# Kernel optimization log

Measured on AMD Instinct MI355X. Metric: run time of the kernel, lower is better.

The kernel has to match this reference:

```python
import jax, jax.numpy as jnp
import numpy as np
from jax import lax

BN_EPS = 1e-5
SQ_EPS = 1e-8


def squash(s, axis=-1):
    # v = (|s|^2 / (1+|s|^2)) * s / |s|
    n2 = jnp.sum(s * s, axis=axis, keepdims=True)
    return (n2 / (1.0 + n2)) * s / jnp.sqrt(n2 + SQ_EPS)


def setup_inputs() -> dict:
    key = jax.random.key(0)
    ks = jax.random.split(key, 5)
    B, C, H, W = 64, 512, 28, 28
    NUM_ROUTES = 8 * 10 * 10  # lower_num_caps * 10 * 10 after k9 s2 conv on 28x28
    features = jax.random.normal(ks[0], (B, C, H, W), jnp.float32)
    conv1_w = jax.random.normal(ks[1], (256, 512, 3, 3), jnp.float32) * 0.02
    conv1_b = jnp.zeros((256,), jnp.float32)
    bn_gamma = jnp.ones((256,), jnp.float32)
    bn_beta = jnp.zeros((256,), jnp.float32)
    bn_mean = jnp.zeros((256,), jnp.float32)
    bn_var = jnp.ones((256,), jnp.float32)
    prim_w = jax.random.normal(ks[2], (256, 256, 9, 9), jnp.float32) * 0.02
    prim_b = jnp.zeros((256,), jnp.float32)
    # routing transform: (num_routes, higher_num_caps, out_dim, in_dim)
    route_w = jax.random.normal(ks[3], (NUM_ROUTES, 2, 16, 32), jnp.float32) * 0.05
    return {"features": features, "conv1_w": conv1_w, "conv1_b": conv1_b,
            "bn_gamma": bn_gamma, "bn_beta": bn_beta, "bn_mean": bn_mean,
            "bn_var": bn_var, "prim_w": prim_w, "prim_b": prim_b,
            "route_w": route_w}


def reference(features, conv1_w, conv1_b, bn_gamma, bn_beta, bn_mean, bn_var,
              prim_w, prim_b, route_w):
    B = features.shape[0]
    dn = ("NCHW", "OIHW", "NCHW")
    # pre_conv: Conv2d(512->256, k3, pad1) + BatchNorm (eval) + ReLU
    x = lax.conv_general_dilated(features, conv1_w, (1, 1), "SAME",
                                 dimension_numbers=dn)
    x = x + conv1_b[None, :, None, None]
    inv = bn_gamma * lax.rsqrt(bn_var + BN_EPS)
    x = x * inv[None, :, None, None] + (bn_beta - bn_mean * inv)[None, :, None, None]
    x = jax.nn.relu(x)
    # primary capsules: Conv2d(256->8*32, k9, s2, valid) -> (B,256,10,10)
    p = lax.conv_general_dilated(x, prim_w, (2, 2), "VALID",
                                 dimension_numbers=dn)
    p = p + prim_b[None, :, None, None]
    Hp, Wp = p.shape[2], p.shape[3]
    # (B, num_caps, cap_dim, Hp*Wp) -> (B, num_caps*Hp*Wp, cap_dim)
    p = p.reshape(B, 8, 32, Hp * Wp).transpose(0, 1, 3, 2).reshape(B, 8 * Hp * Wp, 32)
    lower_caps = squash(p, axis=-1)  # (B, 800, 32)
    # predictions u_hat: (B, routes, higher_caps, out_dim)
    u_hat = jnp.einsum("bri,rjoi->brjo", lower_caps, route_w)
    # dynamic routing-by-agreement
    b = jnp.zeros((B, u_hat.shape[1], u_hat.shape[2]), u_hat.dtype)
    n_iter = 3
    for it in range(n_iter):
        c = jax.nn.softmax(b, axis=2)                  # coupling coeffs
        s = jnp.einsum("brj,brjo->bjo", c, u_hat)      # weighted sum
        v = squash(s, axis=-1)                          # (B, 2, 16)
        if it < n_iter - 1:
            b = b + jnp.einsum("brjo,bjo->brj", u_hat, v)
    return (lower_caps, v)
```

## Files before the change

kernel.cpp:

```cpp
#include <hip/hip_runtime.h>
#include <hip/hip_bf16.h>

#define BN_EPS 1e-5f
#define SQ_EPS 1e-8f

typedef __hip_bfloat16 bf16;
typedef __attribute__((ext_vector_type(8))) short bf16x8;
typedef __attribute__((ext_vector_type(4))) float f32x4;

__device__ __forceinline__ void gload_lds16(const void* g, void* l) {
    __builtin_amdgcn_global_load_lds(
        (const __attribute__((address_space(1))) unsigned int*)g,
        (__attribute__((address_space(3))) unsigned int*)l, 16, 0, 0);
}

__device__ __forceinline__ unsigned short f2bfu(float f) {
    bf16 h = __float2bfloat16(f);
    return *(unsigned short*)&h;
}

__global__ __launch_bounds__(256) void feat_to_nhwc(
    const float* __restrict__ feat, bf16* __restrict__ featP) {
    int b = blockIdx.z, ct = blockIdx.y, pt = blockIdx.x;
    int ci0 = ct * 64, px0 = pt * 64;
    int tid = threadIdx.x;
    __shared__ float t[64][65];
#pragma unroll
    for (int rep = 0; rep < 16; rep++) {
        int ci_l = rep * 4 + (tid >> 6);
        int px = px0 + (tid & 63);
        float v = 0.f;
        if (px < 784) v = feat[(b * 512 + ci0 + ci_l) * 784 + px];
        t[ci_l][tid & 63] = v;
    }
    __syncthreads();
#pragma unroll
    for (int rep = 0; rep < 4; rep++) {
        int px_l = rep * 16 + (tid >> 4);
        int px = px0 + px_l;
        if (px < 784) {
            int h = px / 28, wq = px % 28;
            int ci = (tid & 15) * 4;
            ushort4 o;
            o.x = f2bfu(t[ci + 0][px_l]);
            o.y = f2bfu(t[ci + 1][px_l]);
            o.z = f2bfu(t[ci + 2][px_l]);
            o.w = f2bfu(t[ci + 3][px_l]);
            *(ushort4*)&featP[((b * 30 + h + 1) * 30 + (wq + 1)) * 512 + ci0 + ci] = o;
        }
    }
}

__global__ __launch_bounds__(256) void zero_ring(bf16* __restrict__ featP) {
    int b = blockIdx.x;
    uint4 zz = {0u, 0u, 0u, 0u};
    for (int i = threadIdx.x; i < 116 * 64; i += 256) {
        int rp = i >> 6;
        int ci = (i & 63) * 8;
        int hp, wp;
        if (rp < 30)      { hp = 0;       wp = rp; }
        else if (rp < 60) { hp = 29;      wp = rp - 30; }
        else if (rp < 88) { hp = rp - 59; wp = 0; }
        else              { hp = rp - 87; wp = 29; }
        *(uint4*)&featP[(b * 900 + hp * 30 + wp) * 512 + ci] = zz;
    }
}

__global__ __launch_bounds__(256) void w1F_transform(
    const float* __restrict__ w, bf16* __restrict__ wt1F) {
    int co = blockIdx.x;
    __shared__ float t1[4608];
    const float* src = w + co * 4608;
    for (int i = threadIdx.x; i < 4608; i += 256) t1[i] = src[i];
    __syncthreads();
    int co16 = co >> 4, l15 = co & 15;
    for (int i = threadIdx.x; i < 576; i += 256) {
        int g = i >> 6, cc = (i >> 2) & 15, kq = i & 3;
        short v[8];
#pragma unroll
        for (int j = 0; j < 8; j++) {
            unsigned short u = f2bfu(t1[(cc * 32 + kq * 8 + j) * 9 + g]);
            v[j] = (short)u;
        }
        int fidx = g * 16 + cc;
        bf16x8* dst = (bf16x8*)&wt1F[(fidx * 16 + co16) * 512 + (kq * 16 + l15) * 8];
        bf16x8 pk = {v[0], v[1], v[2], v[3], v[4], v[5], v[6], v[7]};
        *dst = pk;
    }
}

__global__ __launch_bounds__(256) void w2F_transform(
    const float* __restrict__ w, bf16* __restrict__ wt2F) {
    int half = blockIdx.x, co = blockIdx.y;
    __shared__ float t2[10368];
    const float* src = w + co * 20736 + half * 10368;
    for (int i = threadIdx.x; i < 10368; i += 256) t2[i] = src[i];
    __syncthreads();
    int co16 = co >> 4, l15 = co & 15;
    for (int i = threadIdx.x; i < 1296; i += 256) {
        int sh = i >> 4, ccl = (i >> 2) & 3, kq = i & 3;
        int z = sh / 10; if (z > 7) z = 7;
        int s0 = (81 * z) >> 3;
        int fidx = s0 * 8 + (sh - s0) * 8 + (half * 4 + ccl);
        short v[8];
#pragma unroll
        for (int j = 0; j < 8; j++) {
            unsigned short u = f2bfu(t2[(ccl * 32 + kq * 8 + j) * 81 + sh]);
            v[j] = (short)u;
        }
        bf16x8* dst = (bf16x8*)&wt2F[(fidx * 16 + co16) * 512 + (kq * 16 + l15) * 8];
        bf16x8 pk = {v[0], v[1], v[2], v[3], v[4], v[5], v[6], v[7]};
        *dst = pk;
    }
}

__global__ __launch_bounds__(512, 4) void conv1_mfma(
    const bf16* __restrict__ featP, const bf16* __restrict__ wt1F,
    const float* __restrict__ bias, const float* __restrict__ gamma,
    const float* __restrict__ beta, const float* __restrict__ mean,
    const float* __restrict__ var, bf16* __restrict__ x) {
    __shared__ char As4[4 * 7168];
    const int tid = threadIdx.x, lane = tid & 63, w = tid >> 6;
    const int Mt = blockIdx.x;

    const bf16* pA0;
    {
        int r0 = (w << 4) + (lane >> 2);
        int q = (lane & 3) ^ ((r0 >> 1) & 3);
        int m0 = Mt * 112 + (w < 7 ? r0 : 0);
        int b0 = m0 / 784, rr = m0 % 784, h0 = rr / 28, w0 = rr % 28;
        pA0 = featP + ((b0 * 30 + h0) * 30 + w0) * 512 + q * 8;
    }
    const bf16x8* pB = (const bf16x8*)wt1F + w * 128 + lane;

    int a_off[7];
#pragma unroll
    for (int mi = 0; mi < 7; mi++) {
        int r = mi * 16 + (lane & 15);
        a_off[mi] = r * 64 + (((lane >> 4) ^ ((r >> 1) & 3)) * 16);
    }

    f32x4 acc[7][2];
#pragma unroll
    for (int i = 0; i < 7; i++)
#pragma unroll
        for (int j = 0; j < 2; j++) acc[i][j] = f32x4{0.f, 0.f, 0.f, 0.f};

    bf16x8 Bv0[2], Bv1[2];

#define STG1(bi, offE)                                                     \
    do {                                                                   \
        if (w < 7)                                                         \
            gload_lds16(pA0 + (offE), As4 + (bi) * 7168 + w * 1024);       \
    } while (0)

    STG1(0, 0); STG1(1, 32); STG1(2, 64);
    { const bf16x8* bp = pB; Bv0[0] = bp[0]; Bv0[1] = bp[64]; }
    asm volatile("s_waitcnt vmcnt(2)" ::: "memory");
    __builtin_amdgcn_s_barrier();
    asm volatile("" ::: "memory");

#define C1_STEP(u, BU, BL)                                                 \
    do {                                                                   \
        const int t_ = t + (u);                                            \
        const int tt = t_ + 3;                                             \
        {       \
            int g_ = tt >> 4; if (g_ > 8) g_ = 8;                          \
            int cc_ = tt & 15;                                             \
            int ky_ = g_ / 3, kx_ = g_ - 3 * ky_;                          \
            STG1((u + 3) & 3, ky_ * 15360 + kx_ * 512 + cc_ * 32);         \
        }                                                                  \
        {                                                                  \
            int fn = t_ + 1; if (fn > 143) fn = 143;                       \
            const bf16x8* bp = pB + fn * 1024;                             \
            BL[0] = bp[0]; BL[1] = bp[64];                                 \
        }                                                                  \
        const char* Ab = As4 + (u) * 7168;                                 \
        bf16x8 af[7];                                                      \
        _Pragma("unroll")                                                  \
        for (int mi = 0; mi < 7; mi++)                                     \
            af[mi] = *(const bf16x8*)(Ab + a_off[mi]);                     \
        __builtin_amdgcn_s_setprio(1);                                     \
        _Pragma("unroll")                                                  \
        for (int nj = 0; nj < 2; nj++)                                     \
            _Pragma("unroll")                                              \
            for (int mi = 0; mi < 7; mi++)                                 \
                acc[mi][nj] = __builtin_amdgcn_mfma_f32_16x16x32_bf16(     \
                    af[mi], BU[nj], acc[mi][nj], 0, 0, 0);                 \
        __builtin_amdgcn_s_setprio(0);                                     \
        if (t_ < 143) {                                                    \
            asm volatile("s_waitcnt vmcnt(8)" ::: "memory");               \
            __builtin_amdgcn_s_barrier();                                  \
            asm volatile("" ::: "memory");                                 \
        }                                                                  \
    } while (0)

    for (int t = 0; t < 144; t += 4) {
        C1_STEP(0, Bv0, Bv1);
        C1_STEP(1, Bv1, Bv0);
        C1_STEP(2, Bv0, Bv1);
        C1_STEP(3, Bv1, Bv0);
    }

#pragma unroll
    for (int nj = 0; nj < 2; nj++) {
        int co = w * 32 + nj * 16 + (lane & 15);
        float inv = gamma[co] * rsqrtf(var[co] + BN_EPS);
        float sh = beta[co] - mean[co] * inv;
        float bs = bias[co];
#pragma unroll
        for (int mi = 0; mi < 7; mi++) {
            int m0 = Mt * 112 + mi * 16 + ((lane >> 4) << 2);
#pragma unroll
            for (int r = 0; r < 4; r++) {
                float v = (acc[mi][nj][r] + bs) * inv + sh;
                x[(m0 + r) * 256 + co] = __float2bfloat16(fmaxf(v, 0.f));
            }
        }
    }
#undef STG1
#undef C1_STEP
}

__global__ __launch_bounds__(512, 4) void conv2_mfma(
    const bf16* __restrict__ x, const bf16* __restrict__ wt2F,
    bf16* __restrict__ p_parts) {
    __shared__ char As4[4 * 8192];
    const int tid = threadIdx.x, lane = tid & 63, w = tid >> 6;
    const int wr = w >> 2, wc = w & 3;
    const int z = blockIdx.x & 7, Mt = blockIdx.x >> 3;
    const int sh0 = (81 * z) >> 3, sh1 = (81 * (z + 1)) >> 3;
    const int NT = (sh1 - sh0) << 3;
    const int FB = sh0 << 3;

    const bf16* pA0;
    {
        int r0 = (w << 4) + (lane >> 2);
        int q = (lane & 3) ^ ((r0 >> 1) & 3);
        int m0 = Mt * 128 + r0;
        int b0 = m0 / 100, s0 = m0 % 100, ho0 = s0 / 10, wo0 = s0 % 10;
        pA0 = x + ((b0 * 28 + 2 * ho0) * 28 + 2 * wo0) * 256 + q * 8;
    }
    const bf16x8* pB = (const bf16x8*)wt2F + wc * 256 + lane;

    int a_off[4];
#pragma unroll
    for (int mi = 0; mi < 4; mi++) {
        int r = wr * 64 + mi * 16 + (lane & 15);
        a_off[mi] = r * 64 + (((lane >> 4) ^ ((r >> 1) & 3)) * 16);
    }

    f32x4 acc[4][4];
#pragma unroll
    for (int i = 0; i < 4; i++)
#pragma unroll
        for (int j = 0; j < 4; j++) acc[i][j] = f32x4{0.f, 0.f, 0.f, 0.f};

    bf16x8 Bv0[4], Bv1[4];

#define STG2(bi, offE)                                                     \
    gload_lds16(pA0 + (offE), As4 + (bi) * 8192 + w * 1024)

#define A2OFF(tt)                                                          \
    ({ int sh_ = sh0 + ((tt) >> 3); if (sh_ > 80) sh_ = 80;                \
       int cc_ = (tt) & 7;                                                 \
       int ky_ = sh_ / 9, kx_ = sh_ - 9 * ky_;                             \
       (ky_ * 28 + kx_) * 256 + cc_ * 32; })

    STG2(0, A2OFF(0)); STG2(1, A2OFF(1)); STG2(2, A2OFF(2));
    { const bf16x8* bp = pB + FB * 1024;
      Bv0[0] = bp[0]; Bv0[1] = bp[64]; Bv0[2] = bp[128]; Bv0[3] = bp[192]; }
    asm volatile("s_waitcnt vmcnt(4)" ::: "memory");
    __builtin_amdgcn_s_barrier();
    asm volatile("" ::: "memory");

#define C2_STEP(u, BU, BL)                                                 \
    do {                                                                   \
        const int t_ = t + (u);                                            \
        const int tt = t_ + 3;                                             \
        STG2((u + 3) & 3, A2OFF(tt));                                      \
        {                                                                  \
            int fn = t_ + 1; if (fn > NT - 1) fn = NT - 1;                 \
            const bf16x8* bp = pB + (FB + fn) * 1024;                      \
            BL[0] = bp[0]; BL[1] = bp[64];                                 \
            BL[2] = bp[128]; BL[3] = bp[192];                              \
        }                                                                  \
        const char* Ab = As4 + (u) * 8192;                                 \
        __builtin_amdgcn_s_setprio(1);                                     \
        _Pragma("unroll")                                                  \
        for (int mi = 0; mi < 4; mi++) {                                   \
            bf16x8 af = *(const bf16x8*)(Ab + a_off[mi]);                  \
            _Pragma("unroll")                                              \
            for (int nj = 0; nj < 4; nj++)                                 \
                acc[mi][nj] = __builtin_amdgcn_mfma_f32_16x16x32_bf16(     \
                    af, BU[nj], acc[mi][nj], 0, 0, 0);                     \
        }                                                                  \
        __builtin_amdgcn_s_setprio(0);                                     \
        if (t_ < NT - 1) {                                                 \
            asm volatile("s_waitcnt vmcnt(14)" ::: "memory");              \
            __builtin_amdgcn_s_barrier();                                  \
            asm volatile("" ::: "memory");                                 \
        }                                                                  \
    } while (0)

    for (int t = 0; t < NT; t += 4) {
        C2_STEP(0, Bv0, Bv1);
        C2_STEP(1, Bv1, Bv0);
        C2_STEP(2, Bv0, Bv1);
        C2_STEP(3, Bv1, Bv0);
    }

#pragma unroll
    for (int nj = 0; nj < 4; nj++) {
        int co = wc * 64 + nj * 16 + (lane & 15);
#pragma unroll
        for (int mi = 0; mi < 4; mi++) {
            int m0 = Mt * 128 + wr * 64 + mi * 16 + ((lane >> 4) << 2);
#pragma unroll
            for (int r = 0; r < 4; r++)
                p_parts[(z * 6400 + m0 + r) * 256 + co] =
                    __float2bfloat16(acc[mi][nj][r]);
        }
    }
#undef STG2
#undef A2OFF
#undef C2_STEP
}

__global__ __launch_bounds__(256) void squash_kernel(
    const bf16* __restrict__ pp, const float* __restrict__ pb,
    float* __restrict__ lc) {
    int rowg = blockIdx.x * 8 + (threadIdx.x >> 5);
    int i = threadIdx.x & 31;
    int b = rowg / 800, r = rowg - b * 800;
    int cap = r / 100, s = r - cap * 100;
    int m = b * 100 + s, co = cap * 32 + i;
    float val = pb[co];
#pragma unroll
    for (int zz = 0; zz < 8; zz++)
        val += __bfloat162float(pp[(zz * 6400 + m) * 256 + co]);
    float n2 = val * val;
#pragma unroll
    for (int msk = 1; msk < 32; msk <<= 1) n2 += __shfl_xor(n2, msk);
    float scale = n2 / ((1.f + n2) * sqrtf(n2 + SQ_EPS));
    lc[(b * 800 + r) * 32 + i] = val * scale;
}

__global__ __launch_bounds__(256) void uhat_kernel(
    const float* __restrict__ lc, const float* __restrict__ rw,
    bf16* __restrict__ uht) {
    int rT = blockIdx.x, bT = blockIdx.y;
    int rl = threadIdx.x >> 5, jo = threadIdx.x & 31;
    int r = rT * 8 + rl;
    float4 wreg[8];
    const float4* wp4 = reinterpret_cast<const float4*>(rw + (r * 32 + jo) * 32);
#pragma unroll
    for (int k = 0; k < 8; k++) wreg[k] = wp4[k];
    for (int b = bT * 16; b < bT * 16 + 16; b++) {
        const float4* lp4 = reinterpret_cast<const float4*>(lc + (b * 800 + r) * 32);
        float acc = 0.f;
#pragma unroll
        for (int k = 0; k < 8; k++) {
            float4 a = lp4[k];
            acc = fmaf(a.x, wreg[k].x, acc);
            acc = fmaf(a.y, wreg[k].y, acc);
            acc = fmaf(a.z, wreg[k].z, acc);
            acc = fmaf(a.w, wreg[k].w, acc);
        }
        uht[(b * 32 + jo) * 800 + r] = __float2bfloat16(acc);
    }
}

__global__ __launch_bounds__(256) void route_all(
    const bf16* __restrict__ uht, float* __restrict__ vout) {
    extern __shared__ float rs[];
    float* u = rs;
    float* lg = rs + 26400;
    float* red = lg + 1600;
    float* vs = red + 256;
    int b = blockIdx.x, tid = threadIdx.x;
    for (int i = tid; i < 25600; i += 256) {
        int jo = i / 800, r = i - jo * 800;
        u[r * 33 + jo] = __bfloat162float(uht[(b * 32 + jo) * 800 + r]);
    }
    for (int i = tid; i < 1600; i += 256) lg[i] = 0.f;
    __syncthreads();
    int jo = tid & 31, rg = tid >> 5;
    for (int it = 0; it < 3; it++) {
        float sp = 0.f;
        for (int r = rg; r < 800; r += 8) {
            float l0 = lg[r * 2], l1 = lg[r * 2 + 1];
            float m = fmaxf(l0, l1);
            float e0 = __expf(l0 - m), e1 = __expf(l1 - m);
            float c = ((jo < 16) ? e0 : e1) / (e0 + e1);
            sp += c * u[r * 33 + jo];
        }
        red[rg * 32 + jo] = sp;
        __syncthreads();
        if (tid < 32) {
            float s = 0.f;
#pragma unroll
            for (int k = 0; k < 8; k++) s += red[k * 32 + tid];
            float n2 = s * s;
#pragma unroll
            for (int m = 1; m < 16; m <<= 1) n2 += __shfl_xor(n2, m);
            float scale = n2 / ((1.f + n2) * sqrtf(n2 + SQ_EPS));
            float v = s * scale;
            vs[tid] = v;
            if (it == 2) vout[b * 32 + tid] = v;
        }
        __syncthreads();
        if (it < 2) {
            for (int r = tid; r < 800; r += 256) {
                float d0 = 0.f, d1 = 0.f;
#pragma unroll
                for (int o = 0; o < 16; o++) {
                    d0 += u[r * 33 + o] * vs[o];
                    d1 += u[r * 33 + 16 + o] * vs[16 + o];
                }
                lg[r * 2] += d0;
                lg[r * 2 + 1] += d1;
            }
            __syncthreads();
        }
    }
}

extern "C" void kernel_launch(void* const* d_in, const int* in_sizes, int n_in,
                              void* d_out, int out_size, void* d_ws, size_t ws_size,
                              hipStream_t stream) {
    const float* feat    = (const float*)d_in[0];
    const float* conv1_w = (const float*)d_in[1];
    const float* conv1_b = (const float*)d_in[2];
    const float* bn_g    = (const float*)d_in[3];
    const float* bn_b    = (const float*)d_in[4];
    const float* bn_m    = (const float*)d_in[5];
    const float* bn_v    = (const float*)d_in[6];
    const float* prim_w  = (const float*)d_in[7];
    const float* prim_b  = (const float*)d_in[8];
    const float* route_w = (const float*)d_in[9];
    float* out = (float*)d_out;

    char* wsb = (char*)d_ws;
    bf16*  featP   = (bf16*)(wsb + 0);
    bf16*  p_parts = (bf16*)(wsb + 0);
    bf16*  uht     = (bf16*)(wsb + 26214400);
    bf16*  x       = (bf16*)(wsb + 58982400);
    bf16*  wt1F    = (bf16*)(wsb + 84672512);
    bf16*  wt2F    = (bf16*)(wsb + 87031808);

    float* lc_out = out;
    float* v_out  = out + 64 * 800 * 32;

    hipFuncSetAttribute((const void*)route_all,
                        hipFuncAttributeMaxDynamicSharedMemorySize, 113152);

    feat_to_nhwc<<<dim3(13, 8, 64), 256, 0, stream>>>(feat, featP);
    zero_ring<<<64, 256, 0, stream>>>(featP);
    w1F_transform<<<256, 256, 0, stream>>>(conv1_w, wt1F);
    w2F_transform<<<dim3(2, 256), 256, 0, stream>>>(prim_w, wt2F);

    conv1_mfma<<<448, 512, 0, stream>>>(
        featP, wt1F, conv1_b, bn_g, bn_b, bn_m, bn_v, x);

    conv2_mfma<<<400, 512, 0, stream>>>(x, wt2F, p_parts);

    squash_kernel<<<6400, 256, 0, stream>>>(p_parts, prim_b, lc_out);

    uhat_kernel<<<dim3(100, 4), 256, 0, stream>>>(lc_out, route_w, uht);

    route_all<<<64, 256, 113152, stream>>>(uht, v_out);
}
```

Baseline: 336.5 us.

## Halve waves per block in conv kernels, doubling per-wave output tile

Both MFMA conv kernels drop from 8 to 4 waves per block. Each wave now computes a larger register tile (7x4 or 8x4 MFMA fragments) and issues two LDS-staging loads per step instead of one. The intent is to reuse each A fragment across more B columns and cut LDS reads per MFMA and barrier participants. In exchange each wave needs many more accumulator registers, there are fewer waves per CU, and the global-load issue rate per wave doubles, all of which may hurt latency hiding.

```diff
diff --git a/kernel.cpp b/kernel.cpp
--- a/kernel.cpp
+++ b/kernel.cpp
@@ -114,24 +114,31 @@
     }
 }
 
-__global__ __launch_bounds__(512, 4) void conv1_mfma(
+__global__ __launch_bounds__(256, 2) void conv1_mfma(
     const bf16* __restrict__ featP, const bf16* __restrict__ wt1F,
     const float* __restrict__ bias, const float* __restrict__ gamma,
     const float* __restrict__ beta, const float* __restrict__ mean,
     const float* __restrict__ var, bf16* __restrict__ x) {
-    __shared__ char As4[4 * 7168];
+    __shared__ char As4[4 * 8192];
     const int tid = threadIdx.x, lane = tid & 63, w = tid >> 6;
     const int Mt = blockIdx.x;
 
-    const bf16* pA0;
+    const bf16 *pA0, *pA1;
     {
-        int r0 = (w << 4) + (lane >> 2);
-        int q = (lane & 3) ^ ((r0 >> 1) & 3);
-        int m0 = Mt * 112 + (w < 7 ? r0 : 0);
+        int r0 = (w << 5) + (lane >> 2);
+        int r0c = r0 < 112 ? r0 : 111;
+        int q0 = (lane & 3) ^ ((r0c >> 1) & 3);
+        int m0 = Mt * 112 + r0c;
         int b0 = m0 / 784, rr = m0 % 784, h0 = rr / 28, w0 = rr % 28;
-        pA0 = featP + ((b0 * 30 + h0) * 30 + w0) * 512 + q * 8;
-    }
-    const bf16x8* pB = (const bf16x8*)wt1F + w * 128 + lane;
+        pA0 = featP + ((b0 * 30 + h0) * 30 + w0) * 512 + q0 * 8;
+        int r1 = r0 + 16;
+        int r1c = r1 < 112 ? r1 : 111;
+        int q1 = (lane & 3) ^ ((r1c >> 1) & 3);
+        int m1 = Mt * 112 + r1c;
+        int b1 = m1 / 784, rr1 = m1 % 784, h1 = rr1 / 28, w1 = rr1 % 28;
+        pA1 = featP + ((b1 * 30 + h1) * 30 + w1) * 512 + q1 * 8;
+    }
+    const bf16x8* pB = (const bf16x8*)wt1F + w * 256 + lane;
 
     int a_off[7];
 #pragma unroll
@@ -140,23 +147,24 @@
         a_off[mi] = r * 64 + (((lane >> 4) ^ ((r >> 1) & 3)) * 16);
     }
 
-    f32x4 acc[7][2];
+    f32x4 acc[7][4];
 #pragma unroll
     for (int i = 0; i < 7; i++)
 #pragma unroll
-        for (int j = 0; j < 2; j++) acc[i][j] = f32x4{0.f, 0.f, 0.f, 0.f};
-
-    bf16x8 Bv0[2], Bv1[2];
+        for (int j = 0; j < 4; j++) acc[i][j] = f32x4{0.f, 0.f, 0.f, 0.f};
+
+    bf16x8 Bv0[4], Bv1[4];
 
 #define STG1(bi, offE)                                                     \
     do {                                                                   \
-        if (w < 7)                                                         \
-            gload_lds16(pA0 + (offE), As4 + (bi) * 7168 + w * 1024);       \
+        gload_lds16(pA0 + (offE), As4 + (bi) * 8192 + w * 2048);           \
+        gload_lds16(pA1 + (offE), As4 + (bi) * 8192 + w * 2048 + 1024);    \
     } while (0)
 
     STG1(0, 0); STG1(1, 32); STG1(2, 64);
-    { const bf16x8* bp = pB; Bv0[0] = bp[0]; Bv0[1] = bp[64]; }
-    asm volatile("s_waitcnt vmcnt(2)" ::: "memory");
+    { const bf16x8* bp = pB;
+      Bv0[0] = bp[0]; Bv0[1] = bp[64]; Bv0[2] = bp[128]; Bv0[3] = bp[192]; }
+    asm volatile("s_waitcnt vmcnt(8)" ::: "memory");
     __builtin_amdgcn_s_barrier();
     asm volatile("" ::: "memory");
 
@@ -174,22 +182,23 @@
             int fn = t_ + 1; if (fn > 143) fn = 143;                       \
             const bf16x8* bp = pB + fn * 1024;                             \
             BL[0] = bp[0]; BL[1] = bp[64];                                 \
+            BL[2] = bp[128]; BL[3] = bp[192];                              \
         }                                                                  \
-        const char* Ab = As4 + (u) * 7168;                                 \
+        const char* Ab = As4 + (u) * 8192;                                 \
         bf16x8 af[7];                                                      \
         _Pragma("unroll")                                                  \
         for (int mi = 0; mi < 7; mi++)                                     \
             af[mi] = *(const bf16x8*)(Ab + a_off[mi]);                     \
         __builtin_amdgcn_s_setprio(1);                                     \
         _Pragma("unroll")                                                  \
-        for (int nj = 0; nj < 2; nj++)                                     \
+        for (int nj = 0; nj < 4; nj++)                                     \
             _Pragma("unroll")                                              \
             for (int mi = 0; mi < 7; mi++)                                 \
                 acc[mi][nj] = __builtin_amdgcn_mfma_f32_16x16x32_bf16(     \
                     af[mi], BU[nj], acc[mi][nj], 0, 0, 0);                 \
         __builtin_amdgcn_s_setprio(0);                                     \
         if (t_ < 143) {                                                    \
-            asm volatile("s_waitcnt vmcnt(8)" ::: "memory");               \
+            asm volatile("s_waitcnt vmcnt(16)" ::: "memory");              \
             __builtin_amdgcn_s_barrier();                                  \
             asm volatile("" ::: "memory");                                 \
         }                                                                  \
@@ -203,8 +212,8 @@
     }
 
 #pragma unroll
-    for (int nj = 0; nj < 2; nj++) {
-        int co = w * 32 + nj * 16 + (lane & 15);
+    for (int nj = 0; nj < 4; nj++) {
+        int co = w * 64 + nj * 16 + (lane & 15);
         float inv = gamma[co] * rsqrtf(var[co] + BN_EPS);
         float sh = beta[co] - mean[co] * inv;
         float bs = bias[co];
@@ -222,44 +231,51 @@
 #undef C1_STEP
 }
 
-__global__ __launch_bounds__(512, 4) void conv2_mfma(
+__global__ __launch_bounds__(256, 2) void conv2_mfma(
     const bf16* __restrict__ x, const bf16* __restrict__ wt2F,
     bf16* __restrict__ p_parts) {
     __shared__ char As4[4 * 8192];
     const int tid = threadIdx.x, lane = tid & 63, w = tid >> 6;
-    const int wr = w >> 2, wc = w & 3;
     const int z = blockIdx.x & 7, Mt = blockIdx.x >> 3;
     const int sh0 = (81 * z) >> 3, sh1 = (81 * (z + 1)) >> 3;
     const int NT = (sh1 - sh0) << 3;
     const int FB = sh0 << 3;
 
-    const bf16* pA0;
+    const bf16 *pA0, *pA1;
     {
-        int r0 = (w << 4) + (lane >> 2);
-        int q = (lane & 3) ^ ((r0 >> 1) & 3);
+        int r0 = (w << 5) + (lane >> 2);
+        int q0 = (lane & 3) ^ ((r0 >> 1) & 3);
         int m0 = Mt * 128 + r0;
         int b0 = m0 / 100, s0 = m0 % 100, ho0 = s0 / 10, wo0 = s0 % 10;
-        pA0 = x + ((b0 * 28 + 2 * ho0) * 28 + 2 * wo0) * 256 + q * 8;
-    }
-    const bf16x8* pB = (const bf16x8*)wt2F + wc * 256 + lane;
-
-    int a_off[4];
-#pragma unroll
-    for (int mi = 0; mi < 4; mi++) {
-        int r = wr * 64 + mi * 16 + (lane & 15);
+        pA0 = x + ((b0 * 28 + 2 * ho0) * 28 + 2 * wo0) * 256 + q0 * 8;
+        int r1 = r0 + 16;
+        int q1 = (lane & 3) ^ ((r1 >> 1) & 3);
+        int m1 = Mt * 128 + r1;
+        int b1 = m1 / 100, s1 = m1 % 100, ho1 = s1 / 10, wo1 = s1 % 10;
+        pA1 = x + ((b1 * 28 + 2 * ho1) * 28 + 2 * wo1) * 256 + q1 * 8;
+    }
+    const bf16x8* pB = (const bf16x8*)wt2F + w * 256 + lane;
+
+    int a_off[8];
+#pragma unroll
+    for (int mi = 0; mi < 8; mi++) {
+        int r = mi * 16 + (lane & 15);
         a_off[mi] = r * 64 + (((lane >> 4) ^ ((r >> 1) & 3)) * 16);
     }
 
-    f32x4 acc[4][4];
-#pragma unroll
-    for (int i = 0; i < 4; i++)
+    f32x4 acc[8][4];
+#pragma unroll
+    for (int i = 0; i < 8; i++)
 #pragma unroll
         for (int j = 0; j < 4; j++) acc[i][j] = f32x4{0.f, 0.f, 0.f, 0.f};
 
     bf16x8 Bv0[4], Bv1[4];
 
 #define STG2(bi, offE)                                                     \
-    gload_lds16(pA0 + (offE), As4 + (bi) * 8192 + w * 1024)
+    do {                                                                   \
+        gload_lds16(pA0 + (offE), As4 + (bi) * 8192 + w * 2048);           \
+        gload_lds16(pA1 + (offE), As4 + (bi) * 8192 + w * 2048 + 1024);    \
+    } while (0)
 
 #define A2OFF(tt)                                                          \
     ({ int sh_ = sh0 + ((tt) >> 3); if (sh_ > 80) sh_ = 80;                \
@@ -270,7 +286,7 @@
     STG2(0, A2OFF(0)); STG2(1, A2OFF(1)); STG2(2, A2OFF(2));
     { const bf16x8* bp = pB + FB * 1024;
       Bv0[0] = bp[0]; Bv0[1] = bp[64]; Bv0[2] = bp[128]; Bv0[3] = bp[192]; }
-    asm volatile("s_waitcnt vmcnt(4)" ::: "memory");
+    asm volatile("s_waitcnt vmcnt(8)" ::: "memory");
     __builtin_amdgcn_s_barrier();
     asm volatile("" ::: "memory");
 
@@ -286,18 +302,20 @@
             BL[2] = bp[128]; BL[3] = bp[192];                              \
         }                                                                  \
         const char* Ab = As4 + (u) * 8192;                                 \
+        bf16x8 af[8];                                                      \
+        _Pragma("unroll")                                                  \
+        for (int mi = 0; mi < 8; mi++)                                     \
+            af[mi] = *(const bf16x8*)(Ab + a_off[mi]);                     \
         __builtin_amdgcn_s_setprio(1);                                     \
         _Pragma("unroll")                                                  \
-        for (int mi = 0; mi < 4; mi++) {                                   \
-            bf16x8 af = *(const bf16x8*)(Ab + a_off[mi]);                  \
+        for (int nj = 0; nj < 4; nj++)                                     \
             _Pragma("unroll")                                              \
-            for (int nj = 0; nj < 4; nj++)                                 \
+            for (int mi = 0; mi < 8; mi++)                                 \
                 acc[mi][nj] = __builtin_amdgcn_mfma_f32_16x16x32_bf16(     \
-                    af, BU[nj], acc[mi][nj], 0, 0, 0);                     \
-        }                                                                  \
+                    af[mi], BU[nj], acc[mi][nj], 0, 0, 0);                 \
         __builtin_amdgcn_s_setprio(0);                                     \
         if (t_ < NT - 1) {                                                 \
-            asm volatile("s_waitcnt vmcnt(14)" ::: "memory");              \
+            asm volatile("s_waitcnt vmcnt(16)" ::: "memory");              \
             __builtin_amdgcn_s_barrier();                                  \
             asm volatile("" ::: "memory");                                 \
         }                                                                  \
@@ -312,10 +330,10 @@
 
 #pragma unroll
     for (int nj = 0; nj < 4; nj++) {
-        int co = wc * 64 + nj * 16 + (lane & 15);
-#pragma unroll
-        for (int mi = 0; mi < 4; mi++) {
-            int m0 = Mt * 128 + wr * 64 + mi * 16 + ((lane >> 4) << 2);
+        int co = w * 64 + nj * 16 + (lane & 15);
+#pragma unroll
+        for (int mi = 0; mi < 8; mi++) {
+            int m0 = Mt * 128 + mi * 16 + ((lane >> 4) << 2);
 #pragma unroll
             for (int r = 0; r < 4; r++)
                 p_parts[(z * 6400 + m0 + r) * 256 + co] =
@@ -460,10 +478,10 @@
     w1F_transform<<<256, 256, 0, stream>>>(conv1_w, wt1F);
     w2F_transform<<<dim3(2, 256), 256, 0, stream>>>(prim_w, wt2F);
 
-    conv1_mfma<<<448, 512, 0, stream>>>(
+    conv1_mfma<<<448, 256, 0, stream>>>(
         featP, wt1F, conv1_b, bn_g, bn_b, bn_m, bn_v, x);
 
-    conv2_mfma<<<400, 512, 0, stream>>>(x, wt2F, p_parts);
+    conv2_mfma<<<400, 256, 0, stream>>>(x, wt2F, p_parts);
 
     squash_kernel<<<6400, 256, 0, stream>>>(p_parts, prim_b, lc_out);
 
```

Result: faster. 318.1 us (-5.5%).
